# Kernel optimization log

Hardware: AMD Instinct MI355X
Metric: run time of the kernel (lower is better)

Reference implementation:

```python
import jax, jax.numpy as jnp
import numpy as np

KH, KW = 3, 3
STRIDE, PAD, DIL = 1, 1, 1


def setup_inputs() -> dict:
    key = jax.random.key(0)
    k1, k2, k3, k4 = jax.random.split(key, 4)
    B, C, H, W = 4, 256, 64, 64
    O = 256
    x = jax.random.normal(k1, (B, C, H, W), dtype=jnp.float32)
    offset = jax.random.normal(k2, (B, 2 * KH * KW, H, W), dtype=jnp.float32)
    mask = jax.random.uniform(k3, (B, KH * KW, H, W), dtype=jnp.float32)
    weight = jax.random.normal(k4, (O, C, KH, KW), dtype=jnp.float32) * 0.02
    bias = jnp.zeros((O,), dtype=jnp.float32)
    return {"x": x, "offset": offset, "mask": mask, "weight": weight, "bias": bias}


def _bilinear_sample(x, py, px):
    # x: [B,C,H,W]; py,px: [B,K,Ho,Wo] fractional sample coords (zero outside)
    B, C, H, W = x.shape
    y0 = jnp.floor(py)
    x0 = jnp.floor(px)
    ly, lx = py - y0, px - x0
    hy, hx = 1.0 - ly, 1.0 - lx
    y0i = y0.astype(jnp.int32)
    x0i = x0.astype(jnp.int32)
    xf = x.reshape(B, C, H * W)

    def gather(yi, xi):
        valid = (yi >= 0) & (yi < H) & (xi >= 0) & (xi < W)
        yc = jnp.clip(yi, 0, H - 1)
        xc = jnp.clip(xi, 0, W - 1)
        idx = yc * W + xc  # [B,K,Ho,Wo]
        g = jax.vmap(lambda xb, ib: xb[:, ib.reshape(-1)])(xf, idx)  # [B,C,K*Ho*Wo]
        g = g.reshape(B, C, *yi.shape[1:])
        return g * valid[:, None].astype(x.dtype)

    return (gather(y0i, x0i) * (hy * hx)[:, None]
            + gather(y0i, x0i + 1) * (hy * lx)[:, None]
            + gather(y0i + 1, x0i) * (ly * hx)[:, None]
            + gather(y0i + 1, x0i + 1) * (ly * lx)[:, None])


def reference(x, offset, mask, weight, bias):
    B, C, H, W = x.shape
    O = weight.shape[0]
    K = KH * KW
    Ho = (H + 2 * PAD - DIL * (KH - 1) - 1) // STRIDE + 1
    Wo = (W + 2 * PAD - DIL * (KW - 1) - 1) // STRIDE + 1
    off = offset.reshape(B, K, 2, Ho, Wo)
    tap_y = (jnp.repeat(jnp.arange(KH), KW) * DIL).astype(x.dtype)  # [K]
    tap_x = (jnp.tile(jnp.arange(KW), KH) * DIL).astype(x.dtype)
    base_y = (jnp.arange(Ho) * STRIDE - PAD).astype(x.dtype)  # [Ho]
    base_x = (jnp.arange(Wo) * STRIDE - PAD).astype(x.dtype)
    py = off[:, :, 0] + base_y[None, None, :, None] + tap_y[None, :, None, None]
    px = off[:, :, 1] + base_x[None, None, None, :] + tap_x[None, :, None, None]
    # sampled columns: [B,C,K,Ho,Wo], modulated by mask
    val = _bilinear_sample(x, py, px) * mask[:, None]
    out = jnp.einsum('bckhw,ock->bohw', val, weight.reshape(O, C, K))
    return out + bias[None, :, None, None]
```

## Files before the change

kernel.cpp:

```cpp
#include <hip/hip_runtime.h>

typedef _Float16 f16x8 __attribute__((ext_vector_type(8)));
typedef float f32x4 __attribute__((ext_vector_type(4)));

__device__ __forceinline__ unsigned short f2h(float f) {
  union { _Float16 h; unsigned short u; } v;
  v.h = (_Float16)f;
  return v.u;
}
__device__ __forceinline__ f16x8 splat8(float w) {
  _Float16 h = (_Float16)w;
  f16x8 v = {h, h, h, h, h, h, h, h};
  return v;
}

__global__ __launch_bounds__(256) void prep_wx(
    const float* __restrict__ x, const float* __restrict__ w,
    unsigned short* __restrict__ xt, uint4* __restrict__ wfrag) {
  const int bid = blockIdx.x;
  const int t = threadIdx.x;
  if (bid >= 1024) {
    const int idx = (bid - 1024) * 256 + t;
    const int l = idx & 63;
    const int kt = (idx >> 6) % 72;
    const int g = idx / (72 * 64);
    const int o = g * 16 + (l & 15);
    const int kbase = kt * 32 + ((l >> 4) * 8);
    unsigned short h[8];
#pragma unroll
    for (int e = 0; e < 8; ++e) {
      const int klin = kbase + e;
      const int kk = klin >> 8;
      const int c = klin & 255;
      h[e] = f2h(w[((size_t)o * 256 + c) * 9 + kk]);
    }
    uint4 p;
    p.x = (unsigned)h[0] | ((unsigned)h[1] << 16);
    p.y = (unsigned)h[2] | ((unsigned)h[3] << 16);
    p.z = (unsigned)h[4] | ((unsigned)h[5] << 16);
    p.w = (unsigned)h[6] | ((unsigned)h[7] << 16);
    wfrag[idx] = p;
    return;
  }
  const int b = bid >> 8;
  const int h = (bid >> 2) & 63;
  const int cq = bid & 3;
  const int wave = t >> 6, lane = t & 63;
  __shared__ float lds[64][65];
  const int wpos = t >> 2, sub = t & 3;
  const int cl0 = wave * 4 + (lane >> 4);
  const int w0 = (lane & 15) * 4;
#pragma unroll
  for (int iter = 0; iter < 4; ++iter) {
    const int cl = iter * 16 + cl0;
    const int c = cq * 64 + cl;
    float4 v = *(const float4*)(x + (((size_t)b * 256 + c) * 64 + h) * 64 + w0);
    lds[cl][w0] = v.x; lds[cl][w0 + 1] = v.y;
    lds[cl][w0 + 2] = v.z; lds[cl][w0 + 3] = v.w;
  }
  __syncthreads();
  unsigned short hb[16];
#pragma unroll
  for (int j = 0; j < 16; ++j) hb[j] = f2h(lds[sub * 16 + j][wpos]);
  uint4 p0, p1;
  p0.x = (unsigned)hb[0] | ((unsigned)hb[1] << 16);
  p0.y = (unsigned)hb[2] | ((unsigned)hb[3] << 16);
  p0.z = (unsigned)hb[4] | ((unsigned)hb[5] << 16);
  p0.w = (unsigned)hb[6] | ((unsigned)hb[7] << 16);
  p1.x = (unsigned)hb[8] | ((unsigned)hb[9] << 16);
  p1.y = (unsigned)hb[10] | ((unsigned)hb[11] << 16);
  p1.z = (unsigned)hb[12] | ((unsigned)hb[13] << 16);
  p1.w = (unsigned)hb[14] | ((unsigned)hb[15] << 16);
  unsigned short* dst = xt + (((size_t)b * 64 + h) * 64 + wpos) * 256 + cq * 64 + sub * 16;
  *(uint4*)dst = p0;
  *(uint4*)(dst + 8) = p1;
}

__device__ __forceinline__ void combine8(uint4 q0, uint4 q1, uint4 q2, uint4 q3,
                                         float4 wt, _Float16* dst) {
  f16x8 t0, t1, t2, t3;
  __builtin_memcpy(&t0, &q0, 16);
  __builtin_memcpy(&t1, &q1, 16);
  __builtin_memcpy(&t2, &q2, 16);
  __builtin_memcpy(&t3, &q3, 16);
  f16x8 r = t0 * splat8(wt.x);
  r += t1 * splat8(wt.y);
  r += t2 * splat8(wt.z);
  r += t3 * splat8(wt.w);
  __builtin_memcpy(dst, &r, 16);
}

__global__ __launch_bounds__(512, 2) void dcn_fused(
    const unsigned short* __restrict__ xt, const float* __restrict__ off,
    const float* __restrict__ mask, const uint4* __restrict__ wfrag,
    const float* __restrict__ bias, float* __restrict__ out) {
  __shared__ __align__(16) _Float16 Bs[4][4096];
  __shared__ __align__(16) float swt[9 * 64 * 4];
  __shared__ __align__(16) int sidx[9 * 64 * 4];

  const int bid = blockIdx.x;
  const int id = ((bid & 7) << 5) | (bid >> 3);
  const int b = id >> 6;
  const int nt = id & 63;

  const int tid = threadIdx.x;
  const int lane = tid & 63;
  const int wv = tid >> 6;
  const int lh = lane & 15, lg = lane >> 4;

  for (int pair = tid; pair < 576; pair += 512) {
    const int k = pair >> 6;
    const int pl = pair & 63;
    float oy = off[(((size_t)b * 18 + 2 * k) * 64 + nt) * 64 + pl];
    float ox = off[(((size_t)b * 18 + 2 * k + 1) * 64 + nt) * 64 + pl];
    float m = mask[(((size_t)b * 9 + k) * 64 + nt) * 64 + pl];
    float py = oy + (float)(nt - 1 + k / 3);
    float px = ox + (float)(pl - 1 + k % 3);
    float y0f = floorf(py), x0f = floorf(px);
    float ly = py - y0f, lx = px - x0f;
    float hy = 1.f - ly, hx = 1.f - lx;
    int y0 = (int)y0f, x0 = (int)x0f;
    int y1 = y0 + 1, x1 = x0 + 1;
    bool vy0 = (y0 >= 0) && (y0 < 64);
    bool vy1 = (y1 >= 0) && (y1 < 64);
    bool vx0 = (x0 >= 0) && (x0 < 64);
    bool vx1 = (x1 >= 0) && (x1 < 64);
    int yc0 = min(max(y0, 0), 63), yc1 = min(max(y1, 0), 63);
    int xc0 = min(max(x0, 0), 63), xc1 = min(max(x1, 0), 63);
    int* sp = sidx + (k * 64 + pl) * 4;
    float* wp = swt + (k * 64 + pl) * 4;
    sp[0] = (yc0 * 64 + xc0) * 256;
    sp[1] = (yc0 * 64 + xc1) * 256;
    sp[2] = (yc1 * 64 + xc0) * 256;
    sp[3] = (yc1 * 64 + xc1) * 256;
    wp[0] = (vy0 && vx0) ? hy * hx * m : 0.f;
    wp[1] = (vy0 && vx1) ? hy * lx * m : 0.f;
    wp[2] = (vy1 && vx0) ? ly * hx * m : 0.f;
    wp[3] = (vy1 && vx1) ? ly * lx * m : 0.f;
  }

  const uint4* aBase = wfrag + (size_t)(wv * 2) * 72 * 64 + lane;

  const int pos = tid >> 3, ci = tid & 7;
  const unsigned short* xtb = xt + (size_t)b * 1048576 + ci * 8;
  const int bsw = (ci >> 2) * 2048 + pos * 32 + (((ci & 3) ^ ((pos >> 1) & 3)) * 8);

  const int csw = (lg ^ ((lh >> 1) & 3)) * 8;
  int boff[4];
#pragma unroll
  for (int fn = 0; fn < 4; ++fn) boff[fn] = (fn * 16 + lh) * 32 + csw;

#define LOADA(T, AR4)                                                              \
  do {                                                                             \
    _Pragma("unroll") for (int j = 0; j < 4; ++j)                                  \
        (AR4)[j] = aBase[(size_t)((((j & 1) * 72) + 2 * (T) + (j >> 1)) * 64)];    \
  } while (0)

#define LOADTAPS(T, Q0, Q1, Q2, Q3)                                                \
  do {                                                                             \
    int4 ix = *(const int4*)(sidx + (((T) >> 2) * 64 + pos) * 4);                  \
    const int co = ((T) & 3) * 64;                                                 \
    Q0 = *(const uint4*)(xtb + ix.x + co);                                         \
    Q1 = *(const uint4*)(xtb + ix.y + co);                                         \
    Q2 = *(const uint4*)(xtb + ix.z + co);                                         \
    Q3 = *(const uint4*)(xtb + ix.w + co);                                         \
  } while (0)

#define COMBINE(T, Q0, Q1, Q2, Q3)                                                 \
  do {                                                                             \
    float4 wt4 = *(const float4*)(swt + (((T) >> 2) * 64 + pos) * 4);              \
    combine8(Q0, Q1, Q2, Q3, wt4, &Bs[(T) & 3][0] + bsw);                          \
  } while (0)

#define MFMA_T(T, AR4)                                                             \
  do {                                                                             \
    const _Float16* Bb = &Bs[(T) & 3][0];                                          \
    f16x8 b0[4], b1[4];                                                            \
    _Pragma("unroll") for (int fn = 0; fn < 4; ++fn) {                             \
      b0[fn] = *(const f16x8*)(Bb + boff[fn]);                                     \
      b1[fn] = *(const f16x8*)(Bb + 2048 + boff[fn]);                              \
    }                                                                              \
    __builtin_amdgcn_s_setprio(1);                                                 \
    _Pragma("unroll") for (int fm = 0; fm < 2; ++fm)                               \
        _Pragma("unroll") for (int fn = 0; fn < 4; ++fn) {                         \
      acc[fm][fn] = __builtin_amdgcn_mfma_f32_16x16x32_f16(                        \
          *(const f16x8*)&(AR4)[fm], b0[fn], acc[fm][fn], 0, 0, 0);                \
      acc[fm][fn] = __builtin_amdgcn_mfma_f32_16x16x32_f16(                        \
          *(const f16x8*)&(AR4)[2 + fm], b1[fn], acc[fm][fn], 0, 0, 0);            \
    }                                                                              \
    __builtin_amdgcn_s_setprio(0);                                                 \
  } while (0)

#define BAR()                                                                      \
  do {                                                                             \
    asm volatile("s_waitcnt lgkmcnt(0)" ::: "memory");                             \
    __builtin_amdgcn_sched_barrier(0);                                             \
    __builtin_amdgcn_s_barrier();                                                  \
    __builtin_amdgcn_sched_barrier(0);                                             \
  } while (0)

#define SUPER(S_, ACUR, ANXT)                                                      \
  do {                                                                             \
    MFMA_T(2 * (S_), ACUR);                                                        \
    MFMA_T(2 * (S_) + 1, (ACUR) + 4);                                              \
    LOADA(2 * (S_) + 2, ANXT);                                                     \
    LOADA(2 * (S_) + 3, (ANXT) + 4);                                               \
    COMBINE(2 * (S_) + 2, qA0, qA1, qA2, qA3);                                     \
    LOADTAPS(2 * (S_) + 4, qA0, qA1, qA2, qA3);                                    \
    COMBINE(2 * (S_) + 3, qB0, qB1, qB2, qB3);                                     \
    LOADTAPS(2 * (S_) + 5, qB0, qB1, qB2, qB3);                                    \
    BAR();                                                                         \
  } while (0)

  f32x4 acc[2][4] = {};
  uint4 AE[8], AO[8];
  uint4 qA0, qA1, qA2, qA3, qB0, qB1, qB2, qB3;

  __syncthreads();

  {
    LOADTAPS(0, qA0, qA1, qA2, qA3);
    LOADTAPS(1, qB0, qB1, qB2, qB3);
    COMBINE(0, qA0, qA1, qA2, qA3);
    COMBINE(1, qB0, qB1, qB2, qB3);
    LOADA(0, AE);
    LOADA(1, AE + 4);
    LOADTAPS(2, qA0, qA1, qA2, qA3);
    LOADTAPS(3, qB0, qB1, qB2, qB3);
    BAR();
  }

  for (int s = 0; s < 16; s += 2) {
    SUPER(s, AE, AO);
    SUPER(s + 1, AO, AE);
  }
  {
    MFMA_T(32, AE);
    MFMA_T(33, AE + 4);
    LOADA(34, AO);
    LOADA(35, AO + 4);
    COMBINE(34, qA0, qA1, qA2, qA3);
    COMBINE(35, qB0, qB1, qB2, qB3);
    BAR();
  }
  MFMA_T(34, AO);
  MFMA_T(35, AO + 4);

  float* outb = out + (size_t)b * 1048576 + (size_t)nt * 64;
#pragma unroll
  for (int fm = 0; fm < 2; ++fm) {
#pragma unroll
    for (int i = 0; i < 4; ++i) {
      const int o = wv * 32 + fm * 16 + lg * 4 + i;
      const float bs = bias[o];
      float* orow = outb + (size_t)o * 4096 + lh;
#pragma unroll
      for (int fn = 0; fn < 4; ++fn) orow[fn * 16] = acc[fm][fn][i] + bs;
    }
  }
#undef LOADA
#undef LOADTAPS
#undef COMBINE
#undef MFMA_T
#undef BAR
#undef SUPER
}

extern "C" void kernel_launch(void* const* d_in, const int* in_sizes, int n_in,
                              void* d_out, int out_size, void* d_ws, size_t ws_size,
                              hipStream_t stream) {
  const float* x = (const float*)d_in[0];
  const float* off = (const float*)d_in[1];
  const float* mask = (const float*)d_in[2];
  const float* wgt = (const float*)d_in[3];
  const float* bias = (const float*)d_in[4];
  float* out = (float*)d_out;

  uint4* wfrag = (uint4*)d_ws;
  unsigned short* xtp = (unsigned short*)(wfrag + 73728);

  prep_wx<<<1312, 256, 0, stream>>>(x, wgt, xtp, wfrag);
  dcn_fused<<<256, 512, 0, stream>>>(xtp, off, mask, wfrag, bias, out);
}
```

Baseline: 45.25 us.

## Halve spatial tile per block and split K across waves with LDS reduction

```diff
diff --git a/kernel.cpp b/kernel.cpp
--- a/kernel.cpp
+++ b/kernel.cpp
@@ -1,6 +1,7 @@
 #include <hip/hip_runtime.h>
 
 typedef _Float16 f16x8 __attribute__((ext_vector_type(8)));
+typedef _Float16 f16x4 __attribute__((ext_vector_type(4)));
 typedef float f32x4 __attribute__((ext_vector_type(4)));
 
 __device__ __forceinline__ unsigned short f2h(float f) {
@@ -8,9 +9,9 @@
   v.h = (_Float16)f;
   return v.u;
 }
-__device__ __forceinline__ f16x8 splat8(float w) {
+__device__ __forceinline__ f16x4 splat4(float w) {
   _Float16 h = (_Float16)w;
-  f16x8 v = {h, h, h, h, h, h, h, h};
+  f16x4 v = {h, h, h, h};
   return v;
 }
 
@@ -76,46 +77,51 @@
   *(uint4*)(dst + 8) = p1;
 }
 
-__device__ __forceinline__ void combine8(uint4 q0, uint4 q1, uint4 q2, uint4 q3,
+__device__ __forceinline__ void combine4(uint2 q0, uint2 q1, uint2 q2, uint2 q3,
                                          float4 wt, _Float16* dst) {
-  f16x8 t0, t1, t2, t3;
-  __builtin_memcpy(&t0, &q0, 16);
-  __builtin_memcpy(&t1, &q1, 16);
-  __builtin_memcpy(&t2, &q2, 16);
-  __builtin_memcpy(&t3, &q3, 16);
-  f16x8 r = t0 * splat8(wt.x);
-  r += t1 * splat8(wt.y);
-  r += t2 * splat8(wt.z);
-  r += t3 * splat8(wt.w);
-  __builtin_memcpy(dst, &r, 16);
-}
-
-__global__ __launch_bounds__(512, 2) void dcn_fused(
+  f16x4 t0, t1, t2, t3;
+  __builtin_memcpy(&t0, &q0, 8);
+  __builtin_memcpy(&t1, &q1, 8);
+  __builtin_memcpy(&t2, &q2, 8);
+  __builtin_memcpy(&t3, &q3, 8);
+  f16x4 r = t0 * splat4(wt.x);
+  r += t1 * splat4(wt.y);
+  r += t2 * splat4(wt.z);
+  r += t3 * splat4(wt.w);
+  __builtin_memcpy(dst, &r, 8);
+}
+
+__global__ __launch_bounds__(512, 4) void dcn_fused(
     const unsigned short* __restrict__ xt, const float* __restrict__ off,
     const float* __restrict__ mask, const uint4* __restrict__ wfrag,
     const float* __restrict__ bias, float* __restrict__ out) {
-  __shared__ __align__(16) _Float16 Bs[4][4096];
-  __shared__ __align__(16) float swt[9 * 64 * 4];
-  __shared__ __align__(16) int sidx[9 * 64 * 4];
+  __shared__ __align__(16) _Float16 Bs[4][2048];
+  __shared__ __align__(16) float red[8192];
+  __shared__ __align__(16) float swt[9 * 32 * 4];
+  __shared__ __align__(16) int sidx[9 * 32 * 4];
 
   const int bid = blockIdx.x;
-  const int id = ((bid & 7) << 5) | (bid >> 3);
-  const int b = id >> 6;
-  const int nt = id & 63;
+  const int id = ((bid & 7) << 6) | (bid >> 3);
+  const int b = id >> 7;
+  const int nt = (id >> 1) & 63;
+  const int nh = id & 1;
 
   const int tid = threadIdx.x;
   const int lane = tid & 63;
   const int wv = tid >> 6;
+  const int m = wv & 3;
+  const int ksA = wv >> 2;
   const int lh = lane & 15, lg = lane >> 4;
 
-  for (int pair = tid; pair < 576; pair += 512) {
-    const int k = pair >> 6;
-    const int pl = pair & 63;
-    float oy = off[(((size_t)b * 18 + 2 * k) * 64 + nt) * 64 + pl];
-    float ox = off[(((size_t)b * 18 + 2 * k + 1) * 64 + nt) * 64 + pl];
-    float m = mask[(((size_t)b * 9 + k) * 64 + nt) * 64 + pl];
+  if (tid < 288) {
+    const int k = tid / 32;
+    const int pl = tid & 31;
+    const int w = nh * 32 + pl;
+    float oy = off[(((size_t)b * 18 + 2 * k) * 64 + nt) * 64 + w];
+    float ox = off[(((size_t)b * 18 + 2 * k + 1) * 64 + nt) * 64 + w];
+    float mm = mask[(((size_t)b * 9 + k) * 64 + nt) * 64 + w];
     float py = oy + (float)(nt - 1 + k / 3);
-    float px = ox + (float)(pl - 1 + k % 3);
+    float px = ox + (float)(w - 1 + k % 3);
     float y0f = floorf(py), x0f = floorf(px);
     float ly = py - y0f, lx = px - x0f;
     float hy = 1.f - ly, hx = 1.f - lx;
@@ -127,67 +133,65 @@
     bool vx1 = (x1 >= 0) && (x1 < 64);
     int yc0 = min(max(y0, 0), 63), yc1 = min(max(y1, 0), 63);
     int xc0 = min(max(x0, 0), 63), xc1 = min(max(x1, 0), 63);
-    int* sp = sidx + (k * 64 + pl) * 4;
-    float* wp = swt + (k * 64 + pl) * 4;
+    int* sp = sidx + (k * 32 + pl) * 4;
+    float* wp = swt + (k * 32 + pl) * 4;
     sp[0] = (yc0 * 64 + xc0) * 256;
     sp[1] = (yc0 * 64 + xc1) * 256;
     sp[2] = (yc1 * 64 + xc0) * 256;
     sp[3] = (yc1 * 64 + xc1) * 256;
-    wp[0] = (vy0 && vx0) ? hy * hx * m : 0.f;
-    wp[1] = (vy0 && vx1) ? hy * lx * m : 0.f;
-    wp[2] = (vy1 && vx0) ? ly * hx * m : 0.f;
-    wp[3] = (vy1 && vx1) ? ly * lx * m : 0.f;
-  }
-
-  const uint4* aBase = wfrag + (size_t)(wv * 2) * 72 * 64 + lane;
-
-  const int pos = tid >> 3, ci = tid & 7;
-  const unsigned short* xtb = xt + (size_t)b * 1048576 + ci * 8;
-  const int bsw = (ci >> 2) * 2048 + pos * 32 + (((ci & 3) ^ ((pos >> 1) & 3)) * 8);
+    wp[0] = (vy0 && vx0) ? hy * hx * mm : 0.f;
+    wp[1] = (vy0 && vx1) ? hy * lx * mm : 0.f;
+    wp[2] = (vy1 && vx0) ? ly * hx * mm : 0.f;
+    wp[3] = (vy1 && vx1) ? ly * lx * mm : 0.f;
+  }
+
+  const uint4* aBase = wfrag + (size_t)(m * 4) * 4608 + lane;
+
+  const int pos = tid >> 4;
+  const int ci = tid & 15;
+  const unsigned short* xtb = xt + (size_t)b * 1048576 + ci * 4;
+  const int bsw = (ci >> 3) * 1024 + pos * 32 +
+                  ((((ci >> 1) & 3) ^ ((pos >> 1) & 3)) << 3) + ((ci & 1) << 2);
 
   const int csw = (lg ^ ((lh >> 1) & 3)) * 8;
-  int boff[4];
-#pragma unroll
-  for (int fn = 0; fn < 4; ++fn) boff[fn] = (fn * 16 + lh) * 32 + csw;
+  int boff[2];
+#pragma unroll
+  for (int fn = 0; fn < 2; ++fn)
+    boff[fn] = ksA * 1024 + (fn * 16 + lh) * 32 + csw;
 
 #define LOADA(T, AR4)                                                              \
   do {                                                                             \
     _Pragma("unroll") for (int j = 0; j < 4; ++j)                                  \
-        (AR4)[j] = aBase[(size_t)((((j & 1) * 72) + 2 * (T) + (j >> 1)) * 64)];    \
+        (AR4)[j] = aBase[(size_t)(j * 4608 + (2 * (T) + ksA) * 64)];               \
   } while (0)
 
 #define LOADTAPS(T, Q0, Q1, Q2, Q3)                                                \
   do {                                                                             \
-    int4 ix = *(const int4*)(sidx + (((T) >> 2) * 64 + pos) * 4);                  \
+    int4 ix = *(const int4*)(sidx + (((T) >> 2) * 32 + pos) * 4);                  \
     const int co = ((T) & 3) * 64;                                                 \
-    Q0 = *(const uint4*)(xtb + ix.x + co);                                         \
-    Q1 = *(const uint4*)(xtb + ix.y + co);                                         \
-    Q2 = *(const uint4*)(xtb + ix.z + co);                                         \
-    Q3 = *(const uint4*)(xtb + ix.w + co);                                         \
+    Q0 = *(const uint2*)(xtb + ix.x + co);                                         \
+    Q1 = *(const uint2*)(xtb + ix.y + co);                                         \
+    Q2 = *(const uint2*)(xtb + ix.z + co);                                         \
+    Q3 = *(const uint2*)(xtb + ix.w + co);                                         \
   } while (0)
 
 #define COMBINE(T, Q0, Q1, Q2, Q3)                                                 \
   do {                                                                             \
-    float4 wt4 = *(const float4*)(swt + (((T) >> 2) * 64 + pos) * 4);              \
-    combine8(Q0, Q1, Q2, Q3, wt4, &Bs[(T) & 3][0] + bsw);                          \
+    float4 wt4 = *(const float4*)(swt + (((T) >> 2) * 32 + pos) * 4);              \
+    combine4(Q0, Q1, Q2, Q3, wt4, &Bs[(T) & 3][bsw]);                              \
   } while (0)
 
 #define MFMA_T(T, AR4)                                                             \
   do {                                                                             \
     const _Float16* Bb = &Bs[(T) & 3][0];                                          \
-    f16x8 b0[4], b1[4];                                                            \
-    _Pragma("unroll") for (int fn = 0; fn < 4; ++fn) {                             \
-      b0[fn] = *(const f16x8*)(Bb + boff[fn]);                                     \
-      b1[fn] = *(const f16x8*)(Bb + 2048 + boff[fn]);                              \
-    }                                                                              \
+    f16x8 bv[2];                                                                   \
+    _Pragma("unroll") for (int fn = 0; fn < 2; ++fn)                               \
+        bv[fn] = *(const f16x8*)(Bb + boff[fn]);                                   \
     __builtin_amdgcn_s_setprio(1);                                                 \
-    _Pragma("unroll") for (int fm = 0; fm < 2; ++fm)                               \
-        _Pragma("unroll") for (int fn = 0; fn < 4; ++fn) {                         \
-      acc[fm][fn] = __builtin_amdgcn_mfma_f32_16x16x32_f16(                        \
-          *(const f16x8*)&(AR4)[fm], b0[fn], acc[fm][fn], 0, 0, 0);                \
-      acc[fm][fn] = __builtin_amdgcn_mfma_f32_16x16x32_f16(                        \
-          *(const f16x8*)&(AR4)[2 + fm], b1[fn], acc[fm][fn], 0, 0, 0);            \
-    }                                                                              \
+    _Pragma("unroll") for (int fm = 0; fm < 4; ++fm)                               \
+        _Pragma("unroll") for (int fn = 0; fn < 2; ++fn)                           \
+            acc[fm][fn] = __builtin_amdgcn_mfma_f32_16x16x32_f16(                  \
+                *(const f16x8*)&(AR4)[fm], bv[fn], acc[fm][fn], 0, 0, 0);          \
     __builtin_amdgcn_s_setprio(0);                                                 \
   } while (0)
 
@@ -199,71 +203,75 @@
     __builtin_amdgcn_sched_barrier(0);                                             \
   } while (0)
 
-#define SUPER(S_, ACUR, ANXT)                                                      \
-  do {                                                                             \
-    MFMA_T(2 * (S_), ACUR);                                                        \
-    MFMA_T(2 * (S_) + 1, (ACUR) + 4);                                              \
-    LOADA(2 * (S_) + 2, ANXT);                                                     \
-    LOADA(2 * (S_) + 3, (ANXT) + 4);                                               \
-    COMBINE(2 * (S_) + 2, qA0, qA1, qA2, qA3);                                     \
-    LOADTAPS(2 * (S_) + 4, qA0, qA1, qA2, qA3);                                    \
-    COMBINE(2 * (S_) + 3, qB0, qB1, qB2, qB3);                                     \
-    LOADTAPS(2 * (S_) + 5, qB0, qB1, qB2, qB3);                                    \
+#define PHASE(P_, ALT, ACUR, QL0, QL1, QL2, QL3, QC0, QC1, QC2, QC3)               \
+  do {                                                                             \
+    LOADA((P_) + 1, ALT);                                                          \
+    LOADTAPS((P_) + 2, QL0, QL1, QL2, QL3);                                        \
+    COMBINE((P_) + 1, QC0, QC1, QC2, QC3);                                         \
+    MFMA_T((P_), ACUR);                                                            \
     BAR();                                                                         \
   } while (0)
 
-  f32x4 acc[2][4] = {};
-  uint4 AE[8], AO[8];
-  uint4 qA0, qA1, qA2, qA3, qB0, qB1, qB2, qB3;
+  f32x4 acc[4][2] = {};
+  uint4 AE[4], AO[4];
+  uint2 qA0, qA1, qA2, qA3, qB0, qB1, qB2, qB3;
 
   __syncthreads();
 
   {
     LOADTAPS(0, qA0, qA1, qA2, qA3);
+    COMBINE(0, qA0, qA1, qA2, qA3);
+    LOADA(0, AE);
     LOADTAPS(1, qB0, qB1, qB2, qB3);
-    COMBINE(0, qA0, qA1, qA2, qA3);
-    COMBINE(1, qB0, qB1, qB2, qB3);
-    LOADA(0, AE);
-    LOADA(1, AE + 4);
-    LOADTAPS(2, qA0, qA1, qA2, qA3);
-    LOADTAPS(3, qB0, qB1, qB2, qB3);
     BAR();
   }
 
-  for (int s = 0; s < 16; s += 2) {
-    SUPER(s, AE, AO);
-    SUPER(s + 1, AO, AE);
+  for (int p = 0; p < 34; p += 2) {
+    PHASE(p, AO, AE, qA0, qA1, qA2, qA3, qB0, qB1, qB2, qB3);
+    PHASE(p + 1, AE, AO, qB0, qB1, qB2, qB3, qA0, qA1, qA2, qA3);
   }
   {
-    MFMA_T(32, AE);
-    MFMA_T(33, AE + 4);
-    LOADA(34, AO);
-    LOADA(35, AO + 4);
-    COMBINE(34, qA0, qA1, qA2, qA3);
+    LOADA(35, AO);
     COMBINE(35, qB0, qB1, qB2, qB3);
+    MFMA_T(34, AE);
     BAR();
-  }
-  MFMA_T(34, AO);
-  MFMA_T(35, AO + 4);
-
-  float* outb = out + (size_t)b * 1048576 + (size_t)nt * 64;
-#pragma unroll
-  for (int fm = 0; fm < 2; ++fm) {
-#pragma unroll
-    for (int i = 0; i < 4; ++i) {
-      const int o = wv * 32 + fm * 16 + lg * 4 + i;
-      const float bs = bias[o];
-      float* orow = outb + (size_t)o * 4096 + lh;
-#pragma unroll
-      for (int fn = 0; fn < 4; ++fn) orow[fn * 16] = acc[fm][fn][i] + bs;
-    }
+    MFMA_T(35, AO);
+  }
+
+  __syncthreads();
+  if (ksA == 1) {
+    float* rb = red + (size_t)(m * 64 + lane) * 32;
+#pragma unroll
+    for (int fm = 0; fm < 4; ++fm)
+#pragma unroll
+      for (int fn = 0; fn < 2; ++fn) {
+        const int f = fm * 2 + fn;
+        *(f32x4*)(rb + ((f ^ (lane & 7)) * 4)) = acc[fm][fn];
+      }
+  }
+  __syncthreads();
+  if (ksA == 0) {
+    const float* rb = red + (size_t)(m * 64 + lane) * 32;
+    float* outb = out + (size_t)b * 1048576 + (size_t)nt * 64 + nh * 32;
+#pragma unroll
+    for (int fm = 0; fm < 4; ++fm)
+#pragma unroll
+      for (int fn = 0; fn < 2; ++fn) {
+        const int f = fm * 2 + fn;
+        f32x4 v = *(const f32x4*)(rb + ((f ^ (lane & 7)) * 4));
+#pragma unroll
+        for (int i = 0; i < 4; ++i) {
+          const int o = m * 64 + fm * 16 + lg * 4 + i;
+          outb[(size_t)o * 4096 + fn * 16 + lh] = v[i] + acc[fm][fn][i] + bias[o];
+        }
+      }
   }
 #undef LOADA
 #undef LOADTAPS
 #undef COMBINE
 #undef MFMA_T
 #undef BAR
-#undef SUPER
+#undef PHASE
 }
 
 extern "C" void kernel_launch(void* const* d_in, const int* in_sizes, int n_in,
@@ -280,5 +288,5 @@
   unsigned short* xtp = (unsigned short*)(wfrag + 73728);
 
   prep_wx<<<1312, 256, 0, stream>>>(x, wgt, xtp, wfrag);
-  dcn_fused<<<256, 512, 0, stream>>>(xtp, off, mask, wfrag, bias, out);
-}
+  dcn_fused<<<512, 512, 0, stream>>>(xtp, off, mask, wfrag, bias, out);
+}
```

Result: slower. 55.30 us (+22.2%).
